# Performance work log

Hardware: AMD Instinct MI355X
Metric: run time of the kernel (lower is better)

## Reference

```python
import jax, jax.numpy as jnp
import numpy as np

# CrossAttention (DFFNet): 1x1 convs produce q,k from depth and v from rgb;
# full dense attention over hw spatial tokens: softmax(q^T k) then v @ mask^T.

def setup_inputs() -> dict:
    key = jax.random.key(0)
    ks = jax.random.split(key, 8)
    B, C, H, W = 4, 256, 64, 64
    Cqk = C // 8  # ratio=8 -> 32
    s = 0.02
    return {
        "rgb":   jax.random.normal(ks[0], (B, C, H, W), jnp.float32),
        "depth": jax.random.normal(ks[1], (B, C, H, W), jnp.float32),
        "Wq": jax.random.normal(ks[2], (Cqk, C), jnp.float32) * s,
        "bq": jax.random.normal(ks[3], (Cqk,), jnp.float32) * s,
        "Wk": jax.random.normal(ks[4], (Cqk, C), jnp.float32) * s,
        "bk": jax.random.normal(ks[5], (Cqk,), jnp.float32) * s,
        "Wv": jax.random.normal(ks[6], (C, C), jnp.float32) * s,
        "bv": jax.random.normal(ks[7], (C,), jnp.float32) * s,
    }


def reference(rgb, depth, Wq, bq, Wk, bk, Wv, bv):
    B, C, H, W = rgb.shape
    hw = H * W
    d = depth.reshape(B, C, hw)   # [B, C, hw]
    r = rgb.reshape(B, C, hw)     # [B, C, hw]
    # 1x1 convs == channel-mixing linear maps
    q = jnp.einsum('oc,bcn->bon', Wq, d) + bq[None, :, None]  # [B, Cqk, hw]
    k = jnp.einsum('oc,bcn->bon', Wk, d) + bk[None, :, None]  # [B, Cqk, hw]
    v = jnp.einsum('oc,bcn->bon', Wv, r) + bv[None, :, None]  # [B, C, hw]
    # scores: q^T k -> [B, hw, hw], softmax over last dim
    scores = jnp.einsum('bcn,bcm->bnm', q, k)
    mask = jax.nn.softmax(scores, axis=-1)
    # feat = v @ mask^T  -> [B, C, hw]
    feat = jnp.einsum('bcm,bnm->bcn', v, mask)
    return feat.reshape(B, C, H, W)
```

## Files before the change

kernel.cpp:

```cpp
#include <hip/hip_runtime.h>
#include <stdint.h>

#define L2E 1.44269504088896340736f

typedef _Float16 half8 __attribute__((ext_vector_type(8)));
typedef float floatx4 __attribute__((ext_vector_type(4)));

static __device__ __forceinline__ unsigned short f32_to_f16u(float f) {
  union { _Float16 h; unsigned short s; } cv; cv.h = (_Float16)f; return cv.s;
}

static __device__ __forceinline__ float fast_exp2(float x) {
  float r;
  asm("v_exp_f32 %0, %1" : "=v"(r) : "v"(x));
  return r;
}

typedef __attribute__((address_space(3))) unsigned int as3_uint;
typedef __attribute__((address_space(1))) const unsigned int as1_cuint;

static __device__ __forceinline__ void async16(const void* g, void* l) {
  __builtin_amdgcn_global_load_lds((as1_cuint*)g, (as3_uint*)l, 16, 0, 0);
}

__global__ __launch_bounds__(256) void proj_kernel(
    const float* __restrict__ rgb,
    const float* __restrict__ depth,
    const float* __restrict__ Wq, const float* __restrict__ bq,
    const float* __restrict__ Wk, const float* __restrict__ bk,
    const float* __restrict__ Wv, const float* __restrict__ bv,
    unsigned short* __restrict__ qT,
    unsigned short* __restrict__ kT,
    unsigned short* __restrict__ v)
{
  __shared__ __align__(16) unsigned short sX[256 * 76];
  __shared__ __align__(16) unsigned short sW[32 * 256];

  const int n0 = blockIdx.x * 64;
  const int b  = blockIdx.y;
  const int z  = blockIdx.z;
  const int t  = threadIdx.x;
  const int w  = t >> 6;
  const int lane = t & 63;
  const int l15 = lane & 15;
  const int q4  = lane >> 4;

  const float* X = (z == 0) ? depth : rgb;
  const float* xb = X + (size_t)b * 256 * 4096 + n0;

#pragma unroll
  for (int i = 0; i < 8; i++) {
    int h = i * 256 + t;
    int c = h >> 3, oct = h & 7;
    const float* src = xb + (size_t)c * 4096 + oct * 8;
    float4 x0 = *(const float4*)src;
    float4 x1 = *(const float4*)(src + 4);
    half8 hh;
    hh[0] = (_Float16)x0.x; hh[1] = (_Float16)x0.y; hh[2] = (_Float16)x0.z; hh[3] = (_Float16)x0.w;
    hh[4] = (_Float16)x1.x; hh[5] = (_Float16)x1.y; hh[6] = (_Float16)x1.z; hh[7] = (_Float16)x1.w;
    *(half8*)&sX[c * 76 + oct * 8] = hh;
  }
  __syncthreads();

  half8 a8[8];
#pragma unroll
  for (int ks = 0; ks < 8; ks++) {
#pragma unroll
    for (int j = 0; j < 8; j++) {
      a8[ks][j] = *(const _Float16*)&sX[(ks * 32 + q4 * 8 + j) * 76 + 16 * w + l15];
    }
  }

  const int ns = (z == 0) ? 2 : 4;
  for (int s = 0; s < ns; s++) {
    const int colbase = (z == 0) ? 0 : (z - 1) * 128 + s * 32;
    __syncthreads();

#pragma unroll
    for (int i = 0; i < 4; i++) {
      int L = i * 256 + t;
      int og = L >> 5;
      int phys = L & 31;
      int ci = phys ^ (og & 7);
      const float* wr;
      if (z == 0) wr = ((s == 0) ? Wq : Wk) + (size_t)og * 256;
      else        wr = Wv + (size_t)(colbase + og) * 256;
      float4 w0 = *(const float4*)(wr + ci * 8);
      float4 w1 = *(const float4*)(wr + ci * 8 + 4);
      half8 h;
      h[0] = (_Float16)w0.x; h[1] = (_Float16)w0.y; h[2] = (_Float16)w0.z; h[3] = (_Float16)w0.w;
      h[4] = (_Float16)w1.x; h[5] = (_Float16)w1.y; h[6] = (_Float16)w1.z; h[7] = (_Float16)w1.w;
      *(half8*)&sW[(size_t)L * 8] = h;
    }

    float bias2[2];
#pragma unroll
    for (int ct = 0; ct < 2; ct++) {
      int og = ct * 16 + l15;
      if (z == 0) bias2[ct] = (s == 0) ? bq[og] : bk[og];
      else        bias2[ct] = bv[colbase + og];
    }
    __syncthreads();

    floatx4 acc2[2];
    acc2[0] = (floatx4){0.f, 0.f, 0.f, 0.f};
    acc2[1] = (floatx4){0.f, 0.f, 0.f, 0.f};

#pragma unroll
    for (int ks = 0; ks < 8; ks++) {
      const int ci = ks * 4 + q4;
#pragma unroll
      for (int ct = 0; ct < 2; ct++) {
        int og = ct * 16 + l15;
        half8 bf = *(const half8*)&sW[og * 256 + ((ci ^ (og & 7)) * 8)];
        acc2[ct] = __builtin_amdgcn_mfma_f32_16x16x32_f16(a8[ks], bf, acc2[ct], 0, 0, 0);
      }
    }

    __syncthreads();

    if (z == 0) {
#pragma unroll
      for (int ct = 0; ct < 2; ct++) {
        int og = ct * 16 + l15;
#pragma unroll
        for (int r = 0; r < 4; r++) {
          int n = n0 + 16 * w + q4 * 4 + r;
          unsigned short hv = f32_to_f16u(acc2[ct][r] + bias2[ct]);
          if (s == 0) qT[((size_t)b * 4096 + n) * 32 + og] = hv;
          else        kT[((size_t)b * 4096 + n) * 32 + og] = hv;
        }
      }
    } else {
      unsigned short* tile = sW;
#pragma unroll
      for (int ct = 0; ct < 2; ct++) {
#pragma unroll
        for (int r = 0; r < 4; r++) {
          int co_l = ct * 16 + l15;
          int nl = 16 * w + q4 * 4 + r;
          tile[co_l * 72 + nl] = f32_to_f16u(acc2[ct][r] + bias2[ct]);
        }
      }
      __syncthreads();
      {
        int co_l = t >> 3;
        int ch = t & 7;
        int4 val = *(const int4*)&tile[co_l * 72 + ch * 8];
        *(int4*)&v[((size_t)b * 256 + colbase + co_l) * 4096 + n0 + ch * 8] = val;
      }
    }
  }
}

static __device__ __forceinline__ void stage_v(
    const unsigned short* __restrict__ vB, unsigned char* sbase,
    int m0, int t, int w)
{
#pragma unroll
  for (int j = 0; j < 4; j++) {
    int lin = j * 256 + t;
    int c = lin >> 2;
    int p = lin & 3;
    int lc = p ^ ((c >> 1) & 3);
    async16(&vB[(size_t)c * 4096 + m0 + lc * 8], sbase + j * 4096 + w * 1024);
  }
}

__global__ __launch_bounds__(256, 4) void attn_kernel(
    const unsigned short* __restrict__ qT,
    const unsigned short* __restrict__ kT,
    const unsigned short* __restrict__ v,
    unsigned short* __restrict__ Op,
    float* __restrict__ lW)
{
  __shared__ __align__(16) unsigned char smem[36864];

  const int o = blockIdx.x;
  const int n0 = ((o >> 3) & 63) * 64;
  const int p  = (o & 7) | ((o >> 9) << 3);
  const int b  = p & 3;
  const int chunk = p >> 2;
  const int t  = threadIdx.x;
  const int w  = t >> 6;
  const int lane = t & 63;
  const int l15 = lane & 15;
  const int q4  = lane >> 4;

  half8 aq = *(const half8*)(qT + ((size_t)b * 4096 + n0 + 16 * w + l15) * 32 + q4 * 8);

  const unsigned short* vB = v + (size_t)b * 256 * 4096;
  const unsigned short* kL = kT + (size_t)b * 4096 * 32 + (size_t)l15 * 32 + q4 * 8;

  float lsum = 0.f;
  floatx4 acc[16];
#pragma unroll
  for (int ct = 0; ct < 16; ct++) acc[ct] = (floatx4){0.f, 0.f, 0.f, 0.f};
  const floatx4 zf = (floatx4){0.f, 0.f, 0.f, 0.f};

  const int mbase = chunk * 1024;

  stage_v(vB, smem, mbase, t, w);
  half8 kc0 = *(const half8*)(kL + (size_t)mbase * 32);
  half8 kc1 = *(const half8*)(kL + (size_t)(mbase + 16) * 32);

  const bool hiB = (lane & 32) != 0;
  const bool hiA = (lane & 16) != 0;

  for (int it = 0; it < 32; ++it) {
    const int m0 = mbase + it * 32;
    asm volatile("s_waitcnt vmcnt(0)" ::: "memory");
    __builtin_amdgcn_s_barrier();
    asm volatile("" ::: "memory");

    if (it < 31) stage_v(vB, smem + ((~it & 1) << 14), m0 + 32, t, w);

    floatx4 s0 = __builtin_amdgcn_mfma_f32_16x16x32_f16(kc0, aq, zf, 0, 0, 0);
    floatx4 s1 = __builtin_amdgcn_mfma_f32_16x16x32_f16(kc1, aq, zf, 0, 0, 0);
    if (it < 31) {
      kc0 = *(const half8*)(kL + (size_t)(m0 + 32) * 32);
      kc1 = *(const half8*)(kL + (size_t)(m0 + 48) * 32);
    }

    union { half8 h; unsigned int d[4]; } Pu, Qu, Ru;
#pragma unroll
    for (int r = 0; r < 4; r++) {
      float p0 = fast_exp2(s0[r] * L2E);
      float p1 = fast_exp2(s1[r] * L2E);
      lsum += p0 + p1;
      Pu.h[r]     = (_Float16)p0;
      Pu.h[4 + r] = (_Float16)p1;
    }
    {
      unsigned int sx = hiB ? Pu.d[0] : Pu.d[2];
      unsigned int sy = hiB ? Pu.d[1] : Pu.d[3];
      unsigned int rx = __shfl_xor(sx, 32);
      unsigned int ry = __shfl_xor(sy, 32);
      Qu.d[0] = hiB ? rx : Pu.d[0];
      Qu.d[1] = hiB ? ry : Pu.d[1];
      Qu.d[2] = hiB ? Pu.d[2] : rx;
      Qu.d[3] = hiB ? Pu.d[3] : ry;
    }
    {
      unsigned int sx = hiA ? Qu.d[0] : Qu.d[2];
      unsigned int sy = hiA ? Qu.d[1] : Qu.d[3];
      unsigned int rx = __shfl_xor(sx, 16);
      unsigned int ry = __shfl_xor(sy, 16);
      Ru.d[0] = hiA ? rx : Qu.d[0];
      Ru.d[1] = hiA ? ry : Qu.d[1];
      Ru.d[2] = hiA ? Qu.d[2] : rx;
      Ru.d[3] = hiA ? Qu.d[3] : ry;
    }
    half8 pb8 = Ru.h;

    const unsigned short* sVb = (const unsigned short*)(smem + ((it & 1) << 14));
#pragma unroll
    for (int ct = 0; ct < 16; ct++) {
      int co = ct * 16 + l15;
      half8 va8 = *(const half8*)&sVb[co * 32 + ((q4 ^ ((co >> 1) & 3)) * 8)];
      acc[ct] = __builtin_amdgcn_mfma_f32_16x16x32_f16(va8, pb8, acc[ct], 0, 0, 0);
    }
  }

  lsum += __shfl_xor(lsum, 16);
  lsum += __shfl_xor(lsum, 32);
  if (q4 == 0)
    lW[((size_t)chunk * 4 + b) * 4096 + n0 + 16 * w + l15] = lsum;

  unsigned short* sO = (unsigned short*)smem;
  __syncthreads();
#pragma unroll
  for (int ct = 0; ct < 16; ct++) {
#pragma unroll
    for (int r = 0; r < 4; r++) {
      sO[(ct * 16 + q4 * 4 + r) * 72 + 16 * w + l15] = f32_to_f16u(acc[ct][r]);
    }
  }
  __syncthreads();
#pragma unroll
  for (int i = 0; i < 8; i++) {
    int co_l = i * 32 + (t >> 3);
    int ch = t & 7;
    int4 val = *(const int4*)&sO[co_l * 72 + ch * 8];
    *(int4*)&Op[(((size_t)chunk * 4 + b) * 256 + co_l) * 4096 + n0 + ch * 8] = val;
  }
}

__global__ __launch_bounds__(256) void combine_kernel(
    const unsigned short* __restrict__ Op,
    const float* __restrict__ lW,
    float* __restrict__ out)
{
  const int t = threadIdx.x;
  const int b = blockIdx.y;
  const size_t n8 = (size_t)blockIdx.x * 2048 + (size_t)t * 8;
  const int co0 = blockIdx.z * 4;

  float sum[8] = {0.f, 0.f, 0.f, 0.f, 0.f, 0.f, 0.f, 0.f};
#pragma unroll
  for (int ch = 0; ch < 4; ch++) {
    const float* lp = lW + ((size_t)ch * 4 + b) * 4096 + n8;
    float4 a0 = *(const float4*)lp;
    float4 a1 = *(const float4*)(lp + 4);
    sum[0] += a0.x; sum[1] += a0.y; sum[2] += a0.z; sum[3] += a0.w;
    sum[4] += a1.x; sum[5] += a1.y; sum[6] += a1.z; sum[7] += a1.w;
  }
  float rl[8];
#pragma unroll
  for (int i = 0; i < 8; i++) rl[i] = 1.0f / sum[i];

#pragma unroll
  for (int cc = 0; cc < 4; cc++) {
    int co = co0 + cc;
    float o[8] = {0.f, 0.f, 0.f, 0.f, 0.f, 0.f, 0.f, 0.f};
#pragma unroll
    for (int ch = 0; ch < 4; ch++) {
      half8 hv = *(const half8*)&Op[(((size_t)ch * 4 + b) * 256 + co) * 4096 + n8];
#pragma unroll
      for (int i = 0; i < 8; i++) o[i] += (float)hv[i];
    }
    float* op = out + ((size_t)b * 256 + co) * 4096 + n8;
    float4 r0, r1;
    r0.x = o[0] * rl[0]; r0.y = o[1] * rl[1]; r0.z = o[2] * rl[2]; r0.w = o[3] * rl[3];
    r1.x = o[4] * rl[4]; r1.y = o[5] * rl[5]; r1.z = o[6] * rl[6]; r1.w = o[7] * rl[7];
    *(float4*)op = r0;
    *(float4*)(op + 4) = r1;
  }
}

extern "C" void kernel_launch(void* const* d_in, const int* in_sizes, int n_in,
                              void* d_out, int out_size, void* d_ws, size_t ws_size,
                              hipStream_t stream) {
  const float* rgb   = (const float*)d_in[0];
  const float* depth = (const float*)d_in[1];
  const float* Wq    = (const float*)d_in[2];
  const float* bq    = (const float*)d_in[3];
  const float* Wk    = (const float*)d_in[4];
  const float* bk    = (const float*)d_in[5];
  const float* Wv    = (const float*)d_in[6];
  const float* bv    = (const float*)d_in[7];
  float* out = (float*)d_out;

  unsigned short* qT = (unsigned short*)d_ws;
  unsigned short* kT = qT + (size_t)4 * 4096 * 32;
  unsigned short* vW = kT + (size_t)4 * 4096 * 32;
  unsigned short* Op = vW + (size_t)4 * 256 * 4096;
  float* lW = (float*)(Op + (size_t)4 * 4 * 256 * 4096);

  dim3 pg(64, 4, 3);
  proj_kernel<<<pg, 256, 0, stream>>>(rgb, depth, Wq, bq, Wk, bk, Wv, bv, qT, kT, vW);
  attn_kernel<<<dim3(1024, 1, 1), 256, 0, stream>>>(qT, kT, vW, Op, lW);
  dim3 cg(2, 4, 64);
  combine_kernel<<<cg, 256, 0, stream>>>(Op, lW, out);
}
```

Measured before the change: 165.2 us.

## Triple-buffer V tiles and software-pipeline score/exp one step ahead

Moves from double to triple buffering of the V tiles in LDS (48KB shared memory) with prefetch distance two, and computes the QK scores and exp for the next tile while the current PV MFMAs run. Partial vmcnt waits replace the full drain, so global loads overlap further with compute. The cost is higher LDS use and register pressure, and the launch bounds drop to 3 blocks per CU, which lowers occupancy.

```diff
diff --git a/kernel.cpp b/kernel.cpp
--- a/kernel.cpp
+++ b/kernel.cpp
@@ -167,14 +167,14 @@
   }
 }
 
-__global__ __launch_bounds__(256, 4) void attn_kernel(
+__global__ __launch_bounds__(256, 3) void attn_kernel(
     const unsigned short* __restrict__ qT,
     const unsigned short* __restrict__ kT,
     const unsigned short* __restrict__ v,
     unsigned short* __restrict__ Op,
     float* __restrict__ lW)
 {
-  __shared__ __align__(16) unsigned char smem[36864];
+  __shared__ __align__(16) unsigned char smem[49152];
 
   const int o = blockIdx.x;
   const int n0 = ((o >> 3) & 63) * 64;
@@ -199,34 +199,15 @@
   const floatx4 zf = (floatx4){0.f, 0.f, 0.f, 0.f};
 
   const int mbase = chunk * 1024;
-
-  stage_v(vB, smem, mbase, t, w);
-  half8 kc0 = *(const half8*)(kL + (size_t)mbase * 32);
-  half8 kc1 = *(const half8*)(kL + (size_t)(mbase + 16) * 32);
-
   const bool hiB = (lane & 32) != 0;
   const bool hiA = (lane & 16) != 0;
 
-  for (int it = 0; it < 32; ++it) {
-    const int m0 = mbase + it * 32;
-    asm volatile("s_waitcnt vmcnt(0)" ::: "memory");
-    __builtin_amdgcn_s_barrier();
-    asm volatile("" ::: "memory");
-
-    if (it < 31) stage_v(vB, smem + ((~it & 1) << 14), m0 + 32, t, w);
-
-    floatx4 s0 = __builtin_amdgcn_mfma_f32_16x16x32_f16(kc0, aq, zf, 0, 0, 0);
-    floatx4 s1 = __builtin_amdgcn_mfma_f32_16x16x32_f16(kc1, aq, zf, 0, 0, 0);
-    if (it < 31) {
-      kc0 = *(const half8*)(kL + (size_t)(m0 + 32) * 32);
-      kc1 = *(const half8*)(kL + (size_t)(m0 + 48) * 32);
-    }
-
+  auto mk_pb = [&](floatx4 e0, floatx4 e1) -> half8 {
     union { half8 h; unsigned int d[4]; } Pu, Qu, Ru;
 #pragma unroll
     for (int r = 0; r < 4; r++) {
-      float p0 = fast_exp2(s0[r] * L2E);
-      float p1 = fast_exp2(s1[r] * L2E);
+      float p0 = fast_exp2(e0[r] * L2E);
+      float p1 = fast_exp2(e1[r] * L2E);
       lsum += p0 + p1;
       Pu.h[r]     = (_Float16)p0;
       Pu.h[4 + r] = (_Float16)p1;
@@ -251,15 +232,50 @@
       Ru.d[2] = hiA ? Qu.d[2] : rx;
       Ru.d[3] = hiA ? Qu.d[3] : ry;
     }
-    half8 pb8 = Ru.h;
-
-    const unsigned short* sVb = (const unsigned short*)(smem + ((it & 1) << 14));
+    return Ru.h;
+  };
+
+  stage_v(vB, smem, mbase, t, w);
+  half8 ka0 = *(const half8*)(kL + (size_t)mbase * 32);
+  half8 ka1 = *(const half8*)(kL + (size_t)(mbase + 16) * 32);
+  half8 kq0 = *(const half8*)(kL + (size_t)(mbase + 32) * 32);
+  half8 kq1 = *(const half8*)(kL + (size_t)(mbase + 48) * 32);
+  stage_v(vB, smem + 16384, mbase + 32, t, w);
+  asm volatile("s_waitcnt vmcnt(6)" ::: "memory");
+  floatx4 s0 = __builtin_amdgcn_mfma_f32_16x16x32_f16(ka0, aq, zf, 0, 0, 0);
+  floatx4 s1 = __builtin_amdgcn_mfma_f32_16x16x32_f16(ka1, aq, zf, 0, 0, 0);
+  half8 pb8 = mk_pb(s0, s1);
+
+  int b0 = 0, b1 = 16384, b2 = 32768;
+
+  for (int it = 0; it < 32; ++it) {
+    if (it <= 30) asm volatile("s_waitcnt vmcnt(4)" ::: "memory");
+    else          asm volatile("s_waitcnt vmcnt(0)" ::: "memory");
+    __builtin_amdgcn_s_barrier();
+    asm volatile("" ::: "memory");
+
+    floatx4 t0, t1;
+    if (it < 31) {
+      t0 = __builtin_amdgcn_mfma_f32_16x16x32_f16(kq0, aq, zf, 0, 0, 0);
+      t1 = __builtin_amdgcn_mfma_f32_16x16x32_f16(kq1, aq, zf, 0, 0, 0);
+    }
+    if (it < 30) {
+      kq0 = *(const half8*)(kL + (size_t)(mbase + (it + 2) * 32) * 32);
+      kq1 = *(const half8*)(kL + (size_t)(mbase + (it + 2) * 32 + 16) * 32);
+      stage_v(vB, smem + b2, mbase + (it + 2) * 32, t, w);
+    }
+
+    const unsigned short* sVb = (const unsigned short*)(smem + b0);
 #pragma unroll
     for (int ct = 0; ct < 16; ct++) {
       int co = ct * 16 + l15;
       half8 va8 = *(const half8*)&sVb[co * 32 + ((q4 ^ ((co >> 1) & 3)) * 8)];
       acc[ct] = __builtin_amdgcn_mfma_f32_16x16x32_f16(va8, pb8, acc[ct], 0, 0, 0);
     }
+
+    if (it < 31) pb8 = mk_pb(t0, t1);
+
+    int tmp = b0; b0 = b1; b1 = b2; b2 = tmp;
   }
 
   lsum += __shfl_xor(lsum, 16);
```

Measured after the change: 167.1 us. Within noise of the previous version (+1.2%).
